# Kernel optimization log

Hardware: AMD Instinct MI355X
Metric: run time of the kernel (lower is better)

## Reference

```python
import jax, jax.numpy as jnp
import numpy as np

B, N, NFEAT, NHID, NHEADS, NCLASS, K1 = 4, 2048, 256, 64, 4, 32, 256
ALPHA = 0.2      # leaky relu slope
NEG = -9e15      # mask value used by the torch impl


def setup_inputs() -> dict:
    key = jax.random.key(0)
    ks = jax.random.split(key, 16)
    s = 0.05
    return {
        "x": jax.random.normal(ks[0], (B, N, NFEAT), jnp.float32),
        "adj": jax.random.randint(ks[1], (B, N, N), 0, 2).astype(jnp.int32),
        "one_hop_idcs": jax.random.randint(ks[2], (B, K1), 0, N),
        # multi-head GAT layer params (stacked over heads)
        "W": jax.random.normal(ks[3], (NHEADS, NFEAT, NHID), jnp.float32) * s,
        "a1": jax.random.normal(ks[4], (NHEADS, NHID), jnp.float32) * s,  # a[:nhid]
        "a2": jax.random.normal(ks[5], (NHEADS, NHID), jnp.float32) * s,  # a[nhid:]
        # output GAT layer params
        "Wo": jax.random.normal(ks[6], (NHEADS * NHID, NCLASS), jnp.float32) * s,
        "ao1": jax.random.normal(ks[7], (NCLASS,), jnp.float32) * s,
        "ao2": jax.random.normal(ks[8], (NCLASS,), jnp.float32) * s,
        # classifier: Linear(32, nclass) -> PReLU(nclass) -> Linear(nclass, 2)
        "W1": jax.random.normal(ks[9], (NCLASS, NCLASS), jnp.float32) * s,
        "b1": jnp.zeros((NCLASS,), jnp.float32),
        "prelu_w": jnp.full((NCLASS,), 0.25, jnp.float32),
        "W2": jax.random.normal(ks[10], (NCLASS, 2), jnp.float32) * s,
        "b2": jnp.zeros((2,), jnp.float32),
    }


def _gat_heads(x, W, a1, a2, adj):
    """Dense multi-head GAT. e_ij = leakyrelu(a^T [Wh_i || Wh_j]) computed
    as broadcast of two rank-1 projections (no [N,N,2d] concat tensor)."""
    Wh = jnp.einsum('bnf,hfd->bhnd', x, W)                 # [B,H,N,d]
    f1 = jnp.einsum('bhnd,hd->bhn', Wh, a1)                # src term
    f2 = jnp.einsum('bhnd,hd->bhn', Wh, a2)                # dst term
    e = jax.nn.leaky_relu(f1[:, :, :, None] + f2[:, :, None, :], ALPHA)
    e = jnp.where(adj[:, None, :, :] > 0, e, NEG)
    attn = jax.nn.softmax(e, axis=-1)                      # [B,H,N,N]
    h = jnp.einsum('bhnm,bhmd->bhnd', attn, Wh)            # [B,H,N,d]
    h = jax.nn.elu(h)                                      # concat=True -> elu
    # concat heads: [B,N,H*d]
    return h.transpose(0, 2, 1, 3).reshape(x.shape[0], x.shape[1], -1)


def _gat_out(x, Wo, ao1, ao2, adj):
    Wh = x @ Wo                                            # [B,N,nclass]
    f1 = Wh @ ao1
    f2 = Wh @ ao2
    e = jax.nn.leaky_relu(f1[:, :, None] + f2[:, None, :], ALPHA)
    e = jnp.where(adj > 0, e, NEG)
    attn = jax.nn.softmax(e, axis=-1)
    return attn @ Wh                                       # concat=False -> no elu here


def reference(x, adj, one_hop_idcs, W, a1, a2, Wo, ao1, ao2,
              W1, b1, prelu_w, W2, b2):
    h = _gat_heads(x, W, a1, a2, adj)          # [B,N,H*nhid]
    h = jax.nn.elu(_gat_out(h, Wo, ao1, ao2, adj))  # [B,N,nclass]
    # vectorized per-batch gather (replaces python loop over b)
    ef = jnp.take_along_axis(h, one_hop_idcs[:, :, None], axis=1)  # [B,K1,nclass]
    ef = ef.reshape(-1, h.shape[-1])
    y = ef @ W1 + b1
    y = jnp.where(y > 0, y, prelu_w * y)       # PReLU(nclass)
    return y @ W2 + b2                         # [B*K1, 2]
```

## Files before the change

### kernel.cpp

```cpp
#include <hip/hip_runtime.h>
#include <hip/hip_bf16.h>
#include <stdint.h>
#include <math.h>

#define BB 4
#define NN 2048
#define NFEAT 256
#define NHID 64
#define NHEADS 4
#define NCLASS 32
#define KK1 256
#define ALPHA 0.2f
#define LOG2E 1.4426950408889634f

typedef _Float16 f16x8 __attribute__((ext_vector_type(8)));
typedef _Float16 f16x4 __attribute__((ext_vector_type(4)));
typedef _Float16 h16x2 __attribute__((ext_vector_type(2)));
typedef float f32x4 __attribute__((ext_vector_type(4)));

__device__ __forceinline__ f16x8 ld8(const _Float16* p){
  f16x8 r;
  *(f16x4*)&r = *(const f16x4*)p;
  *((f16x4*)&r + 1) = *(const f16x4*)(p + 4);
  return r;
}

__device__ __forceinline__ h16x2 pk2(float a, float b){
  auto v = __builtin_amdgcn_cvt_pkrtz(a, b);
  h16x2 r;
  __builtin_memcpy(&r, &v, sizeof(r));
  return r;
}

__device__ __forceinline__ float fexp2(float x){
#if __has_builtin(__builtin_amdgcn_exp2f)
  return __builtin_amdgcn_exp2f(x);
#else
  return exp2f(x);
#endif
}

__global__ void __launch_bounds__(256) pack_adj(const int* __restrict__ adj,
                                                unsigned long long* __restrict__ bits,
                                                int* __restrict__ cnt){
  __shared__ int csum[4];
  int row = blockIdx.x;
  const int* arow = adj + (size_t)row * NN;
  int lane = threadIdx.x & 63, wv = threadIdx.x >> 6;
  int c = 0;
  #pragma unroll
  for (int it=0; it<NN/256; ++it){
    int j = it*256 + threadIdx.x;
    unsigned long long m = __ballot(arow[j] > 0);
    if (lane==0){ bits[(size_t)row*(NN/64) + it*4 + wv] = m; c += __popcll(m); }
  }
  if (lane==0) csum[wv] = c;
  __syncthreads();
  if (threadIdx.x==0) cnt[row] = csum[0]+csum[1]+csum[2]+csum[3];
}

__global__ void __launch_bounds__(256) wh_proj2(const float* __restrict__ x,
        const float* __restrict__ W, const float* __restrict__ a1, const float* __restrict__ a2,
        _Float16* __restrict__ whT, float* __restrict__ f1l, float* __restrict__ f2l){
  __shared__ __align__(16) float xs[64*65];
  __shared__ float red1[4][64];
  __shared__ float red2[4][64];
  int bh = blockIdx.x >> 5;
  int i0 = (blockIdx.x & 31) * 64;
  int b = bh >> 2, h = bh & 3;
  int tid = threadIdx.x;
  int lane = tid & 63;
  int dbase = __builtin_amdgcn_readfirstlane(tid >> 6) * 16;
  float acc[16];
  #pragma unroll
  for (int dd=0; dd<16; ++dd) acc[dd] = 0.f;
  for (int kc=0; kc<4; ++kc){
    int kb = kc*64;
    __syncthreads();
    #pragma unroll
    for (int t=0; t<4; ++t){
      int row = t*16 + (tid>>4);
      int f4 = (tid&15)*4;
      float4 v = *(const float4*)(x + ((size_t)(b*NN + i0 + row))*NFEAT + kb + f4);
      xs[row*65 + f4 + 0] = v.x;
      xs[row*65 + f4 + 1] = v.y;
      xs[row*65 + f4 + 2] = v.z;
      xs[row*65 + f4 + 3] = v.w;
    }
    __syncthreads();
    const float* Wb = W + (size_t)h*NFEAT*NHID + (size_t)kb*NHID + dbase;
    #pragma unroll 4
    for (int f=0; f<64; ++f){
      float xv = xs[lane*65 + f];
      const float* wr = Wb + f*NHID;
      #pragma unroll
      for (int dd=0; dd<16; ++dd) acc[dd] = fmaf(xv, wr[dd], acc[dd]);
    }
  }
  float p1 = 0.f, p2 = 0.f;
  #pragma unroll
  for (int dd=0; dd<16; ++dd){
    int d = dbase + dd;
    whT[((size_t)bh*NHID + d)*NN + i0 + lane] = (_Float16)acc[dd];
    p1 = fmaf(acc[dd], a1[h*NHID + d], p1);
    p2 = fmaf(acc[dd], a2[h*NHID + d], p2);
  }
  int wv = tid >> 6;
  red1[wv][lane] = p1;
  red2[wv][lane] = p2;
  __syncthreads();
  if (tid < 64){
    float s1 = red1[0][tid]+red1[1][tid]+red1[2][tid]+red1[3][tid];
    float s2 = red2[0][tid]+red2[1][tid]+red2[2][tid]+red2[3][tid];
    f1l[(size_t)bh*NN + i0 + tid] = s1 * LOG2E;
    f2l[(size_t)bh*NN + i0 + tid] = s2 * LOG2E;
  }
}

__global__ void __launch_bounds__(256) attn_l1(
        const unsigned long long* __restrict__ bits,
        const _Float16* __restrict__ whT,
        const float* __restrict__ f1l, const float* __restrict__ f2l,
        const int* __restrict__ cnt_in,
        float* __restrict__ pc, float* __restrict__ pl){
  const int JC = 128, PITCH = 132;
  __shared__ __align__(16) _Float16 whs[64*PITCH];
  __shared__ __align__(16) _Float16 wts[32*PITCH];
  int blk = blockIdx.x;
  int js = blk & 1;
  int tile = (blk >> 1) & 63;
  int bh = blk >> 7;
  int b = bh >> 2, h = bh & 3;
  int i0 = tile*32;
  int tid = threadIdx.x;
  int lane = tid & 63, wv = tid >> 6;
  int q = lane >> 4, col = lane & 15;
  int r = tid >> 3, jg = (tid & 7) * 16;
  float f1r = f1l[(size_t)bh*NN + i0 + r];
  bool czr = (cnt_in[b*NN + i0 + r] == 0);
  const unsigned short* mrow = (const unsigned short*)(bits + ((size_t)(b*NN + i0 + r))*(NN/64));
  const float* f2p = f2l + (size_t)bh*NN;
  const _Float16* whg = whT + (size_t)bh*NHID*NN;
  float lacc = 0.f;
  f32x4 c0 = {0.f,0.f,0.f,0.f}, c1 = {0.f,0.f,0.f,0.f};
  for (int ii=0; ii<8; ++ii){
    int it = js*8 + ii;
    __syncthreads();
    #pragma unroll
    for (int dd=0; dd<4; ++dd){
      int d = (tid>>4) + dd*16;
      int j8 = (tid&15)*8;
      uint4 v = *(const uint4*)(whg + (size_t)d*NN + it*JC + j8);
      uint2* w2 = (uint2*)&whs[d*PITCH + j8];
      w2[0] = uint2{v.x, v.y};
      w2[1] = uint2{v.z, v.w};
    }
    {
      unsigned int m16 = mrow[it*8 + (tid&7)];
      const float* fp = f2p + it*JC + jg;
      float4 fa = *(const float4*)(fp);
      float4 fb = *(const float4*)(fp+4);
      float4 fc = *(const float4*)(fp+8);
      float4 fd = *(const float4*)(fp+12);
      float fv[16] = {fa.x,fa.y,fa.z,fa.w, fb.x,fb.y,fb.z,fb.w,
                      fc.x,fc.y,fc.z,fc.w, fd.x,fd.y,fd.z,fd.w};
      h16x2 wp[8];
      #pragma unroll
      for (int p=0; p<8; ++p){
        float s0 = f1r + fv[2*p];
        float s1 = f1r + fv[2*p+1];
        float w0 = fexp2(fmaxf(s0, ALPHA*s0));
        float w1 = fexp2(fmaxf(s1, ALPHA*s1));
        unsigned mb0 = (unsigned)(((int)(m16 << (31 - 2*p))) >> 31);
        unsigned mb1 = (unsigned)(((int)(m16 << (30 - 2*p))) >> 31);
        w0 = __uint_as_float(__float_as_uint(w0) & mb0);
        w1 = __uint_as_float(__float_as_uint(w1) & mb1);
        lacc += w0 + w1;
        wp[p] = pk2(w0, w1);
      }
      if (__builtin_expect(czr, 0)){
        h16x2 one2 = {(_Float16)1.f, (_Float16)1.f};
        #pragma unroll
        for (int p=0; p<8; ++p) wp[p] = one2;
      }
      uint2* wdst = (uint2*)&wts[r*PITCH + jg];
      const uint2* wsrc = (const uint2*)&wp[0];
      wdst[0]=wsrc[0]; wdst[1]=wsrc[1]; wdst[2]=wsrc[2]; wdst[3]=wsrc[3];
    }
    __syncthreads();
    #pragma unroll
    for (int ks=0; ks<4; ++ks){
      int kb = ks*32 + q*8;
      f16x8 a0 = ld8(&wts[col*PITCH + kb]);
      f16x8 a1v = ld8(&wts[(16+col)*PITCH + kb]);
      f16x8 bv = ld8(&whs[(wv*16+col)*PITCH + kb]);
      c0 = __builtin_amdgcn_mfma_f32_16x16x32_f16(a0, bv, c0, 0, 0, 0);
      c1 = __builtin_amdgcn_mfma_f32_16x16x32_f16(a1v, bv, c1, 0, 0, 0);
    }
  }
  lacc += __shfl_xor(lacc, 1, 64);
  lacc += __shfl_xor(lacc, 2, 64);
  lacc += __shfl_xor(lacc, 4, 64);
  float* plh = pl + (size_t)js*BB*NHEADS*NN;
  if ((tid & 7) == 0) plh[(size_t)bh*NN + i0 + r] = czr ? (float)(NN/2) : lacc;
  float* pch = pc + (size_t)js*BB*NN*(NHEADS*NHID);
  int dloc = wv*16 + col;
  #pragma unroll
  for (int mt=0; mt<2; ++mt){
    #pragma unroll
    for (int reg=0; reg<4; ++reg){
      int ir = mt*16 + q*4 + reg;
      pch[((size_t)(b*NN + i0 + ir))*(NHEADS*NHID) + h*NHID + dloc] =
          (mt==0 ? c0[reg] : c1[reg]);
    }
  }
}

__global__ void __launch_bounds__(256) combine_h1(const float* __restrict__ pc,
        const float* __restrict__ pl, float* __restrict__ h1){
  const float* pa = pc;
  const float* pb = pc + (size_t)BB*NN*(NHEADS*NHID);
  const float* la = pl;
  const float* lb = pl + (size_t)BB*NHEADS*NN;
  int row = blockIdx.x*8 + (threadIdx.x>>5);
  int c = (threadIdx.x & 31) * 8;
  int b = row >> 11, i = row & (NN-1);
  int h = c >> 6;
  size_t idx = (size_t)row*(NHEADS*NHID) + c;
  float l = la[((size_t)(b*NHEADS + h))*NN + i] + lb[((size_t)(b*NHEADS + h))*NN + i];
  float il = 1.f / l;
  float4 a0 = *(const float4*)(pa + idx);
  float4 a1 = *(const float4*)(pa + idx + 4);
  float4 b0 = *(const float4*)(pb + idx);
  float4 b1 = *(const float4*)(pb + idx + 4);
  float v[8] = {a0.x+b0.x, a0.y+b0.y, a0.z+b0.z, a0.w+b0.w,
                a1.x+b1.x, a1.y+b1.y, a1.z+b1.z, a1.w+b1.w};
  #pragma unroll
  for (int k=0; k<8; ++k){
    float t = v[k] * il;
    v[k] = t > 0.f ? t : expm1f(t);
  }
  *(float4*)(h1 + idx)     = float4{v[0],v[1],v[2],v[3]};
  *(float4*)(h1 + idx + 4) = float4{v[4],v[5],v[6],v[7]};
}

__global__ void __launch_bounds__(256) out_proj2(const float* __restrict__ h1,
        const float* __restrict__ Wo, const float* __restrict__ ao1, const float* __restrict__ ao2,
        _Float16* __restrict__ whT2, float* __restrict__ f1ol, float* __restrict__ f2ol){
  __shared__ __align__(16) float xs[64*65];
  __shared__ float red1[4][64];
  __shared__ float red2[4][64];
  int b = blockIdx.x >> 5;
  int i0 = (blockIdx.x & 31) * 64;
  int tid = threadIdx.x;
  int lane = tid & 63;
  int dbase = __builtin_amdgcn_readfirstlane(tid >> 6) * 8;
  float acc[8];
  #pragma unroll
  for (int dd=0; dd<8; ++dd) acc[dd] = 0.f;
  for (int kc=0; kc<4; ++kc){
    int kb = kc*64;
    __syncthreads();
    #pragma unroll
    for (int t=0; t<4; ++t){
      int row = t*16 + (tid>>4);
      int f4 = (tid&15)*4;
      float4 v = *(const float4*)(h1 + ((size_t)(b*NN + i0 + row))*256 + kb + f4);
      xs[row*65 + f4 + 0] = v.x;
      xs[row*65 + f4 + 1] = v.y;
      xs[row*65 + f4 + 2] = v.z;
      xs[row*65 + f4 + 3] = v.w;
    }
    __syncthreads();
    #pragma unroll 4
    for (int f=0; f<64; ++f){
      float xv = xs[lane*65 + f];
      const float* wr = Wo + (size_t)(kb+f)*NCLASS + dbase;
      #pragma unroll
      for (int dd=0; dd<8; ++dd) acc[dd] = fmaf(xv, wr[dd], acc[dd]);
    }
  }
  float p1 = 0.f, p2 = 0.f;
  #pragma unroll
  for (int dd=0; dd<8; ++dd){
    int d = dbase + dd;
    whT2[((size_t)b*NCLASS + d)*NN + i0 + lane] = (_Float16)acc[dd];
    p1 = fmaf(acc[dd], ao1[d], p1);
    p2 = fmaf(acc[dd], ao2[d], p2);
  }
  int wv = tid >> 6;
  red1[wv][lane] = p1;
  red2[wv][lane] = p2;
  __syncthreads();
  if (tid < 64){
    float s1 = red1[0][tid]+red1[1][tid]+red1[2][tid]+red1[3][tid];
    float s2 = red2[0][tid]+red2[1][tid]+red2[2][tid]+red2[3][tid];
    f1ol[(size_t)b*NN + i0 + tid] = s1 * LOG2E;
    f2ol[(size_t)b*NN + i0 + tid] = s2 * LOG2E;
  }
}

__global__ void __launch_bounds__(256) attn_l2(
        const unsigned long long* __restrict__ bits,
        const _Float16* __restrict__ whT2,
        const float* __restrict__ f1ol, const float* __restrict__ f2ol,
        const int* __restrict__ cnt_in, const int* __restrict__ oh,
        float* __restrict__ pc, float* __restrict__ pl){
  const int JC = 128, PITCH = 132;
  __shared__ __align__(16) _Float16 whs[32*PITCH];
  __shared__ __align__(16) _Float16 wts[32*PITCH];
  int blk = blockIdx.x;
  int js = blk & 7, kt = (blk>>3) & 7, b = blk >> 6;
  int tid = threadIdx.x;
  int lane = tid & 63, wv = tid >> 6;
  int q = lane >> 4, col = lane & 15;
  int r = tid >> 3, jg = (tid & 7) * 16;
  int row_i = oh[b*KK1 + kt*32 + r];
  float f1r = f1ol[b*NN + row_i];
  bool czr = (cnt_in[b*NN + row_i] == 0);
  const unsigned short* mrow = (const unsigned short*)(bits + ((size_t)(b*NN + row_i))*(NN/64));
  const float* f2p = f2ol + (size_t)b*NN;
  const _Float16* whg = whT2 + (size_t)b*NCLASS*NN;
  float lacc = 0.f;
  f32x4 c0 = {0.f,0.f,0.f,0.f};
  int mt = wv & 1, nt = wv >> 1;
  for (int ii=0; ii<2; ++ii){
    int it = js*2 + ii;
    __syncthreads();
    #pragma unroll
    for (int dd=0; dd<2; ++dd){
      int d = (tid>>4) + dd*16;
      int j8 = (tid&15)*8;
      uint4 v = *(const uint4*)(whg + (size_t)d*NN + it*JC + j8);
      uint2* w2 = (uint2*)&whs[d*PITCH + j8];
      w2[0] = uint2{v.x, v.y};
      w2[1] = uint2{v.z, v.w};
    }
    {
      unsigned int m16 = mrow[it*8 + (tid&7)];
      const float* fp = f2p + it*JC + jg;
      float4 fa = *(const float4*)(fp);
      float4 fb = *(const float4*)(fp+4);
      float4 fc = *(const float4*)(fp+8);
      float4 fd = *(const float4*)(fp+12);
      float fv[16] = {fa.x,fa.y,fa.z,fa.w, fb.x,fb.y,fb.z,fb.w,
                      fc.x,fc.y,fc.z,fc.w, fd.x,fd.y,fd.z,fd.w};
      h16x2 wp[8];
      #pragma unroll
      for (int p=0; p<8; ++p){
        float s0 = f1r + fv[2*p];
        float s1 = f1r + fv[2*p+1];
        s0 = (m16 & (1u<<(2*p)))   ? s0 : -1e5f;
        s1 = (m16 & (1u<<(2*p+1))) ? s1 : -1e5f;
        float e0 = fmaxf(s0, ALPHA*s0);
        float e1 = fmaxf(s1, ALPHA*s1);
        float w0 = exp2f(e0);
        float w1 = exp2f(e1);
        lacc += w0 + w1;
        wp[p] = pk2(w0, w1);
      }
      if (__builtin_expect(czr, 0)){
        h16x2 one2 = {(_Float16)1.f, (_Float16)1.f};
        #pragma unroll
        for (int p=0; p<8; ++p) wp[p] = one2;
        lacc += 16.f;
      }
      uint2* wdst = (uint2*)&wts[r*PITCH + jg];
      const uint2* wsrc = (const uint2*)&wp[0];
      wdst[0]=wsrc[0]; wdst[1]=wsrc[1]; wdst[2]=wsrc[2]; wdst[3]=wsrc[3];
    }
    __syncthreads();
    #pragma unroll
    for (int ks=0; ks<4; ++ks){
      int kb = ks*32 + q*8;
      f16x8 a0 = ld8(&wts[(mt*16+col)*PITCH + kb]);
      f16x8 bv = ld8(&whs[(nt*16+col)*PITCH + kb]);
      c0 = __builtin_amdgcn_mfma_f32_16x16x32_f16(a0, bv, c0, 0, 0, 0);
    }
  }
  lacc += __shfl_xor(lacc, 1, 64);
  lacc += __shfl_xor(lacc, 2, 64);
  lacc += __shfl_xor(lacc, 4, 64);
  if ((tid & 7) == 0) pl[blk*32 + r] = lacc;
  int dloc = nt*16 + col;
  #pragma unroll
  for (int reg=0; reg<4; ++reg){
    int ir = mt*16 + q*4 + reg;
    pc[(size_t)blk*1024 + ir*32 + dloc] = c0[reg];
  }
}

__global__ void __launch_bounds__(256) classify2(const float* __restrict__ pc,
        const float* __restrict__ pl,
        const float* __restrict__ W1, const float* __restrict__ b1,
        const float* __restrict__ pw, const float* __restrict__ W2, const float* __restrict__ b2,
        float* __restrict__ out){
  __shared__ float efs[4][32];
  int wv = threadIdx.x >> 6;
  int lane = threadIdx.x & 63;
  int row = blockIdx.x*4 + wv;
  int b = row >> 8, k = row & 255;
  int kt = k >> 5, r = k & 31;
  int base = (b*8 + kt)*8;
  if (lane < 32){
    float s = 0.f, l = 0.f;
    #pragma unroll
    for (int js=0; js<8; ++js){
      s += pc[(size_t)(base+js)*1024 + r*32 + lane];
      l += pl[(base+js)*32 + r];
    }
    float v = s / l;
    v = v > 0.f ? v : expm1f(v);
    efs[wv][lane] = v;
  }
  __syncthreads();
  const float* ef = efs[wv];
  int c = lane & 31;
  float y = b1[c];
  #pragma unroll 8
  for (int kk=0; kk<32; ++kk) y += ef[kk] * W1[kk*32 + c];
  y = y > 0.f ? y : pw[c]*y;
  float o0 = y * W2[c*2+0];
  float o1 = y * W2[c*2+1];
  #pragma unroll
  for (int o=16;o>0;o>>=1){ o0 += __shfl_xor(o0,o,64); o1 += __shfl_xor(o1,o,64); }
  if (lane==0){ out[row*2+0] = o0 + b2[0]; out[row*2+1] = o1 + b2[1]; }
}

extern "C" void kernel_launch(void* const* d_in, const int* in_sizes, int n_in,
                              void* d_out, int out_size, void* d_ws, size_t ws_size,
                              hipStream_t stream) {
  const float* x    = (const float*)d_in[0];
  const int*   adj  = (const int*)  d_in[1];
  const int*   oh   = (const int*)  d_in[2];
  const float* W    = (const float*)d_in[3];
  const float* a1   = (const float*)d_in[4];
  const float* a2   = (const float*)d_in[5];
  const float* Wo   = (const float*)d_in[6];
  const float* ao1  = (const float*)d_in[7];
  const float* ao2  = (const float*)d_in[8];
  const float* W1   = (const float*)d_in[9];
  const float* b1   = (const float*)d_in[10];
  const float* pw   = (const float*)d_in[11];
  const float* W2   = (const float*)d_in[12];
  const float* b2   = (const float*)d_in[13];
  float* out = (float*)d_out;

  char* base = (char*)d_ws;
  size_t off = 0;
  auto alloc = [&](size_t bytes)->char*{
    char* p = base + off;
    off = (off + bytes + 255) & ~(size_t)255;
    return p;
  };
  unsigned long long* adjbits = (unsigned long long*)alloc((size_t)BB*NN*(NN/64)*8);
  int*   cnt1 = (int*)  alloc((size_t)BB*NN*4);
  _Float16* WhT  = (_Float16*)alloc((size_t)BB*NHEADS*NHID*NN*2);
  float* f1l  = (float*)alloc((size_t)BB*NHEADS*NN*4);
  float* f2l  = (float*)alloc((size_t)BB*NHEADS*NN*4);
  float* h1   = (float*)alloc((size_t)BB*NN*(NHEADS*NHID)*4);
  float* pc1  = (float*)alloc((size_t)2*BB*NN*(NHEADS*NHID)*4);
  float* pl1  = (float*)alloc((size_t)2*BB*NHEADS*NN*4);
  _Float16* WhT2 = (_Float16*)alloc((size_t)BB*NCLASS*NN*2);
  float* f1ol = (float*)alloc((size_t)BB*NN*4);
  float* f2ol = (float*)alloc((size_t)BB*NN*4);
  float* pc   = (float*)alloc((size_t)256*1024*4);
  float* pl   = (float*)alloc((size_t)256*32*4);

  pack_adj<<<BB*NN, 256, 0, stream>>>(adj, adjbits, cnt1);
  wh_proj2<<<BB*NHEADS*(NN/64), 256, 0, stream>>>(x, W, a1, a2, WhT, f1l, f2l);
  attn_l1<<<BB*NHEADS*(NN/32)*2, 256, 0, stream>>>(adjbits, WhT, f1l, f2l, cnt1, pc1, pl1);
  combine_h1<<<(BB*NN)/8, 256, 0, stream>>>(pc1, pl1, h1);
  out_proj2<<<BB*(NN/64), 256, 0, stream>>>(h1, Wo, ao1, ao2, WhT2, f1ol, f2ol);
  attn_l2<<<BB*8*8, 256, 0, stream>>>(adjbits, WhT2, f1ol, f2ol, cnt1, oh, pc, pl);
  classify2<<<(BB*KK1)/4, 256, 0, stream>>>(pc, pl, W1, b1, pw, W2, b2, out);
}
```

Before: 237.6 us.

## Factor attention exp into per-node exponentials and fuse combine into output projection

Layer-1 attention weights exp2(leakyrelu(f1+f2)) are rewritten as max(exp2(f1)*exp2(f2), exp2(a*f1)*exp2(a*f2)), with the four per-node exponentials precomputed in the projection kernel. This removes the per-edge exp2 from the hot attention loop. It doubles the per-column f2 data loaded and can overflow or underflow in fp32 when the logits are large. The combine_h1 kernel is also folded into out_proj2, which now sums the two split-K partials, normalises and applies ELU while staging into LDS, dropping one launch and the h1 round trip.

```diff
diff --git a/kernel.cpp b/kernel.cpp
--- a/kernel.cpp
+++ b/kernel.cpp
@@ -32,14 +32,6 @@
   return r;
 }
 
-__device__ __forceinline__ float fexp2(float x){
-#if __has_builtin(__builtin_amdgcn_exp2f)
-  return __builtin_amdgcn_exp2f(x);
-#else
-  return exp2f(x);
-#endif
-}
-
 __global__ void __launch_bounds__(256) pack_adj(const int* __restrict__ adj,
                                                 unsigned long long* __restrict__ bits,
                                                 int* __restrict__ cnt){
@@ -61,7 +53,7 @@
 
 __global__ void __launch_bounds__(256) wh_proj2(const float* __restrict__ x,
         const float* __restrict__ W, const float* __restrict__ a1, const float* __restrict__ a2,
-        _Float16* __restrict__ whT, float* __restrict__ f1l, float* __restrict__ f2l){
+        _Float16* __restrict__ whT, float2* __restrict__ tu1, float2* __restrict__ tu2){
   __shared__ __align__(16) float xs[64*65];
   __shared__ float red1[4][64];
   __shared__ float red2[4][64];
@@ -112,15 +104,16 @@
   if (tid < 64){
     float s1 = red1[0][tid]+red1[1][tid]+red1[2][tid]+red1[3][tid];
     float s2 = red2[0][tid]+red2[1][tid]+red2[2][tid]+red2[3][tid];
-    f1l[(size_t)bh*NN + i0 + tid] = s1 * LOG2E;
-    f2l[(size_t)bh*NN + i0 + tid] = s2 * LOG2E;
+    float e1 = s1 * LOG2E, e2 = s2 * LOG2E;
+    tu1[(size_t)bh*NN + i0 + tid] = float2{exp2f(e1), exp2f(ALPHA*e1)};
+    tu2[(size_t)bh*NN + i0 + tid] = float2{exp2f(e2), exp2f(ALPHA*e2)};
   }
 }
 
 __global__ void __launch_bounds__(256) attn_l1(
         const unsigned long long* __restrict__ bits,
         const _Float16* __restrict__ whT,
-        const float* __restrict__ f1l, const float* __restrict__ f2l,
+        const float2* __restrict__ tu1, const float2* __restrict__ tu2,
         const int* __restrict__ cnt_in,
         float* __restrict__ pc, float* __restrict__ pl){
   const int JC = 128, PITCH = 132;
@@ -136,10 +129,11 @@
   int lane = tid & 63, wv = tid >> 6;
   int q = lane >> 4, col = lane & 15;
   int r = tid >> 3, jg = (tid & 7) * 16;
-  float f1r = f1l[(size_t)bh*NN + i0 + r];
+  float2 t1p = tu1[(size_t)bh*NN + i0 + r];
+  float t1r = t1p.x, u1r = t1p.y;
   bool czr = (cnt_in[b*NN + i0 + r] == 0);
   const unsigned short* mrow = (const unsigned short*)(bits + ((size_t)(b*NN + i0 + r))*(NN/64));
-  const float* f2p = f2l + (size_t)bh*NN;
+  const float2* tu2p = tu2 + (size_t)bh*NN;
   const _Float16* whg = whT + (size_t)bh*NHID*NN;
   float lacc = 0.f;
   f32x4 c0 = {0.f,0.f,0.f,0.f}, c1 = {0.f,0.f,0.f,0.f};
@@ -157,20 +151,16 @@
     }
     {
       unsigned int m16 = mrow[it*8 + (tid&7)];
-      const float* fp = f2p + it*JC + jg;
-      float4 fa = *(const float4*)(fp);
-      float4 fb = *(const float4*)(fp+4);
-      float4 fc = *(const float4*)(fp+8);
-      float4 fd = *(const float4*)(fp+12);
-      float fv[16] = {fa.x,fa.y,fa.z,fa.w, fb.x,fb.y,fb.z,fb.w,
-                      fc.x,fc.y,fc.z,fc.w, fd.x,fd.y,fd.z,fd.w};
+      const float4* qp = (const float4*)(tu2p + it*JC + jg);
+      float4 qv[8];
+      #pragma unroll
+      for (int k=0; k<8; ++k) qv[k] = qp[k];
       h16x2 wp[8];
       #pragma unroll
       for (int p=0; p<8; ++p){
-        float s0 = f1r + fv[2*p];
-        float s1 = f1r + fv[2*p+1];
-        float w0 = fexp2(fmaxf(s0, ALPHA*s0));
-        float w1 = fexp2(fmaxf(s1, ALPHA*s1));
+        float4 qq = qv[p];
+        float w0 = fmaxf(t1r*qq.x, u1r*qq.y);
+        float w1 = fmaxf(t1r*qq.z, u1r*qq.w);
         unsigned mb0 = (unsigned)(((int)(m16 << (31 - 2*p))) >> 31);
         unsigned mb1 = (unsigned)(((int)(m16 << (30 - 2*p))) >> 31);
         w0 = __uint_as_float(__float_as_uint(w0) & mb0);
@@ -216,35 +206,8 @@
   }
 }
 
-__global__ void __launch_bounds__(256) combine_h1(const float* __restrict__ pc,
-        const float* __restrict__ pl, float* __restrict__ h1){
-  const float* pa = pc;
-  const float* pb = pc + (size_t)BB*NN*(NHEADS*NHID);
-  const float* la = pl;
-  const float* lb = pl + (size_t)BB*NHEADS*NN;
-  int row = blockIdx.x*8 + (threadIdx.x>>5);
-  int c = (threadIdx.x & 31) * 8;
-  int b = row >> 11, i = row & (NN-1);
-  int h = c >> 6;
-  size_t idx = (size_t)row*(NHEADS*NHID) + c;
-  float l = la[((size_t)(b*NHEADS + h))*NN + i] + lb[((size_t)(b*NHEADS + h))*NN + i];
-  float il = 1.f / l;
-  float4 a0 = *(const float4*)(pa + idx);
-  float4 a1 = *(const float4*)(pa + idx + 4);
-  float4 b0 = *(const float4*)(pb + idx);
-  float4 b1 = *(const float4*)(pb + idx + 4);
-  float v[8] = {a0.x+b0.x, a0.y+b0.y, a0.z+b0.z, a0.w+b0.w,
-                a1.x+b1.x, a1.y+b1.y, a1.z+b1.z, a1.w+b1.w};
-  #pragma unroll
-  for (int k=0; k<8; ++k){
-    float t = v[k] * il;
-    v[k] = t > 0.f ? t : expm1f(t);
-  }
-  *(float4*)(h1 + idx)     = float4{v[0],v[1],v[2],v[3]};
-  *(float4*)(h1 + idx + 4) = float4{v[4],v[5],v[6],v[7]};
-}
-
-__global__ void __launch_bounds__(256) out_proj2(const float* __restrict__ h1,
+__global__ void __launch_bounds__(256) out_proj2(const float* __restrict__ pa,
+        const float* __restrict__ pb, const float* __restrict__ la, const float* __restrict__ lb,
         const float* __restrict__ Wo, const float* __restrict__ ao1, const float* __restrict__ ao2,
         _Float16* __restrict__ whT2, float* __restrict__ f1ol, float* __restrict__ f2ol){
   __shared__ __align__(16) float xs[64*65];
@@ -265,11 +228,19 @@
     for (int t=0; t<4; ++t){
       int row = t*16 + (tid>>4);
       int f4 = (tid&15)*4;
-      float4 v = *(const float4*)(h1 + ((size_t)(b*NN + i0 + row))*256 + kb + f4);
-      xs[row*65 + f4 + 0] = v.x;
-      xs[row*65 + f4 + 1] = v.y;
-      xs[row*65 + f4 + 2] = v.z;
-      xs[row*65 + f4 + 3] = v.w;
+      int i = i0 + row;
+      size_t lidx = ((size_t)(b*NHEADS + kc))*NN + i;
+      float l = la[lidx] + lb[lidx];
+      float il = 1.f / l;
+      size_t idx = ((size_t)(b*NN + i))*256 + kb + f4;
+      float4 va = *(const float4*)(pa + idx);
+      float4 vb = *(const float4*)(pb + idx);
+      float v[4] = {(va.x+vb.x)*il, (va.y+vb.y)*il, (va.z+vb.z)*il, (va.w+vb.w)*il};
+      #pragma unroll
+      for (int k=0; k<4; ++k){
+        float t2 = v[k];
+        xs[row*65 + f4 + k] = t2 > 0.f ? t2 : expm1f(t2);
+      }
     }
     __syncthreads();
     #pragma unroll 4
@@ -456,9 +427,8 @@
   unsigned long long* adjbits = (unsigned long long*)alloc((size_t)BB*NN*(NN/64)*8);
   int*   cnt1 = (int*)  alloc((size_t)BB*NN*4);
   _Float16* WhT  = (_Float16*)alloc((size_t)BB*NHEADS*NHID*NN*2);
-  float* f1l  = (float*)alloc((size_t)BB*NHEADS*NN*4);
-  float* f2l  = (float*)alloc((size_t)BB*NHEADS*NN*4);
-  float* h1   = (float*)alloc((size_t)BB*NN*(NHEADS*NHID)*4);
+  float2* tu1 = (float2*)alloc((size_t)BB*NHEADS*NN*8);
+  float2* tu2 = (float2*)alloc((size_t)BB*NHEADS*NN*8);
   float* pc1  = (float*)alloc((size_t)2*BB*NN*(NHEADS*NHID)*4);
   float* pl1  = (float*)alloc((size_t)2*BB*NHEADS*NN*4);
   _Float16* WhT2 = (_Float16*)alloc((size_t)BB*NCLASS*NN*2);
@@ -467,11 +437,15 @@
   float* pc   = (float*)alloc((size_t)256*1024*4);
   float* pl   = (float*)alloc((size_t)256*32*4);
 
+  float* pa = pc1;
+  float* pb = pc1 + (size_t)BB*NN*(NHEADS*NHID);
+  float* la = pl1;
+  float* lb = pl1 + (size_t)BB*NHEADS*NN;
+
   pack_adj<<<BB*NN, 256, 0, stream>>>(adj, adjbits, cnt1);
-  wh_proj2<<<BB*NHEADS*(NN/64), 256, 0, stream>>>(x, W, a1, a2, WhT, f1l, f2l);
-  attn_l1<<<BB*NHEADS*(NN/32)*2, 256, 0, stream>>>(adjbits, WhT, f1l, f2l, cnt1, pc1, pl1);
-  combine_h1<<<(BB*NN)/8, 256, 0, stream>>>(pc1, pl1, h1);
-  out_proj2<<<BB*(NN/64), 256, 0, stream>>>(h1, Wo, ao1, ao2, WhT2, f1ol, f2ol);
+  wh_proj2<<<BB*NHEADS*(NN/64), 256, 0, stream>>>(x, W, a1, a2, WhT, tu1, tu2);
+  attn_l1<<<BB*NHEADS*(NN/32)*2, 256, 0, stream>>>(adjbits, WhT, tu1, tu2, cnt1, pc1, pl1);
+  out_proj2<<<BB*(NN/64), 256, 0, stream>>>(pa, pb, la, lb, Wo, ao1, ao2, WhT2, f1ol, f2ol);
   attn_l2<<<BB*8*8, 256, 0, stream>>>(adjbits, WhT2, f1ol, f2ol, cnt1, oh, pc, pl);
   classify2<<<(BB*KK1)/4, 256, 0, stream>>>(pc, pl, W1, b1, pw, W2, b2, out);
 }
```

Result: slower. 271.5 us (+14.3%).
